# Kernel optimization log

Measured on AMD Instinct MI355X. Metric: run time of the kernel, lower is better.

The kernel has to match this reference:

```python
import jax, jax.numpy as jnp
import numpy as np

N, NFEAT, NHID, NCLASS, NHEAD = 8192, 512, 64, 16, 4
ALPHA = 0.1  # leaky relu slope
NEG = -9e15


def setup_inputs() -> dict:
    key = jax.random.key(0)
    ks = jax.random.split(key, 7)
    x = jax.random.normal(ks[0], (N, NFEAT), dtype=jnp.float32)
    adj = (jax.random.uniform(ks[1], (N, N)) < 0.05).astype(jnp.float32)
    # per-head params: W [H, nfeat, nhid], a [H, 2*nhid] (xavier-ish scale)
    W = jax.random.normal(ks[2], (NHEAD, NFEAT, NHID), dtype=jnp.float32) * (1.0 / np.sqrt(NFEAT))
    a = jax.random.normal(ks[3], (NHEAD, 2 * NHID), dtype=jnp.float32) * (1.0 / np.sqrt(NHID))
    W_out = jax.random.normal(ks[4], (NHEAD * NHID, NCLASS), dtype=jnp.float32) * (1.0 / np.sqrt(NHEAD * NHID))
    a_out = jax.random.normal(ks[5], (2 * NCLASS,), dtype=jnp.float32) * (1.0 / np.sqrt(NCLASS))
    return {"x": x, "adj": adj, "W": W, "a": a, "W_out": W_out, "a_out": a_out}


def _gat_layer(h, adj, Wk, ak):
    """Dense pyGAT GraphAttentionLayer (eval mode, dropout = identity)."""
    d = Wk.shape[1]
    Wh = h @ Wk                         # [N, d]
    f1 = Wh @ ak[:d]                    # [N]
    f2 = Wh @ ak[d:]                    # [N]
    e = jax.nn.leaky_relu(f1[:, None] + f2[None, :], negative_slope=ALPHA)  # [N, N]
    att = jax.nn.softmax(jnp.where(adj > 0, e, NEG), axis=1)
    return att @ Wh                     # [N, d]


def reference(x, adj, W, a, W_out, a_out):
    # eval mode: F.dropout is identity
    heads = jax.vmap(lambda Wk, ak: jax.nn.elu(_gat_layer(x, adj, Wk, ak)))(W, a)  # [H, N, nhid]
    h = jnp.transpose(heads, (1, 0, 2)).reshape(x.shape[0], -1)                    # [N, H*nhid]
    out = jax.nn.elu(_gat_layer(h, adj, W_out, a_out))                             # [N, nclass]
    return jax.nn.log_softmax(out, axis=1)
```

## Files before the change

### kernel.cpp

```cpp
#include <hip/hip_runtime.h>
#include <hip/hip_bf16.h>

#define NN 8192
#define NFEAT 512
#define NHID 64
#define NCLASS 16
#define NHEAD 4
#define ALPHA 0.1f
#define CAP 768

typedef short bf16x8 __attribute__((ext_vector_type(8)));
typedef float f32x4 __attribute__((ext_vector_type(4)));
typedef float fv4 __attribute__((ext_vector_type(4)));

__device__ __forceinline__ float lrelu(float x) { return fmaxf(x, ALPHA * x); }
__device__ __forceinline__ float elu(float x) { return x > 0.f ? x : __expf(x) - 1.f; }
__device__ __forceinline__ short f2b(float x) {
  union { __bf16 b; short s; } c; c.b = (__bf16)x; return c.s;
}
__device__ __forceinline__ float b2f(short x) {
  union { unsigned int u; float f; } c; c.u = ((unsigned int)(unsigned short)x) << 16; return c.f;
}

#define UPF(w, v, A0, A1)                                  \
  {                                                        \
    const float lo_ = __uint_as_float((v) << 16);          \
    const float hi_ = __uint_as_float((v) & 0xffff0000u);  \
    (A0) += (w) * lo_;                                     \
    (A1) += (w) * hi_;                                     \
  }

__global__ __launch_bounds__(256) void k_wprep(const float* __restrict__ W,
                                               short* __restrict__ WB) {
  __shared__ float t[64][65];
  const int h = blockIdx.y;
  const int k0 = blockIdx.x * 64;
  const int tid = threadIdx.x;
#pragma unroll
  for (int it = 0; it < 16; ++it) {
    const int r = it * 4 + (tid >> 6), c = tid & 63;
    t[r][c] = W[((size_t)h * NFEAT + k0 + r) * NHID + c];
  }
  __syncthreads();
#pragma unroll
  for (int it = 0; it < 16; ++it) {
    const int d = it * 4 + (tid >> 6), k = tid & 63;
    WB[((size_t)h * NHID + d) * NFEAT + k0 + k] = f2b(t[k][d]);
  }
}

__global__ __launch_bounds__(256) void k_prep1(const float* __restrict__ x,
                                               const short* __restrict__ WB,
                                               const float* __restrict__ a,
                                               short* __restrict__ Whf,
                                               float* __restrict__ f1i,
                                               float* __restrict__ f2i) {
  __shared__ short tile[64][72];
  const int bid = blockIdx.x;
  const int h = bid >> 7;
  const int bm = (bid & 127) * 64;
  const int tid = threadIdx.x;
  const int wv = tid >> 6, lane = tid & 63;
  const int mr = lane & 15, kg = lane >> 4;
  f32x4 acc0 = {0.f, 0.f, 0.f, 0.f}, acc1 = acc0, acc2 = acc0, acc3 = acc0;
  const float* ap = x + (size_t)(bm + wv * 16 + mr) * NFEAT + kg * 8;
  const short* bp = WB + ((size_t)h * NHID + mr) * NFEAT + kg * 8;
#pragma unroll 2
  for (int k0 = 0; k0 < NFEAT; k0 += 32) {
    const float4 xa = *reinterpret_cast<const float4*>(ap);
    const float4 xb = *reinterpret_cast<const float4*>(ap + 4);
    bf16x8 af;
    af[0] = f2b(xa.x); af[1] = f2b(xa.y); af[2] = f2b(xa.z); af[3] = f2b(xa.w);
    af[4] = f2b(xb.x); af[5] = f2b(xb.y); af[6] = f2b(xb.z); af[7] = f2b(xb.w);
    const bf16x8 b0 = *reinterpret_cast<const bf16x8*>(bp);
    const bf16x8 b1 = *reinterpret_cast<const bf16x8*>(bp + 16 * NFEAT);
    const bf16x8 b2 = *reinterpret_cast<const bf16x8*>(bp + 32 * NFEAT);
    const bf16x8 b3 = *reinterpret_cast<const bf16x8*>(bp + 48 * NFEAT);
    acc0 = __builtin_amdgcn_mfma_f32_16x16x32_bf16(af, b0, acc0, 0, 0, 0);
    acc1 = __builtin_amdgcn_mfma_f32_16x16x32_bf16(af, b1, acc1, 0, 0, 0);
    acc2 = __builtin_amdgcn_mfma_f32_16x16x32_bf16(af, b2, acc2, 0, 0, 0);
    acc3 = __builtin_amdgcn_mfma_f32_16x16x32_bf16(af, b3, acc3, 0, 0, 0);
    ap += 32; bp += 32;
  }
  float a1v[4], a2v[4];
#pragma unroll
  for (int c = 0; c < 4; ++c) {
    a1v[c] = a[h * 128 + mr + c * 16];
    a2v[c] = a[h * 128 + 64 + mr + c * 16];
  }
#pragma unroll
  for (int q = 0; q < 4; ++q) {
    float s1 = acc0[q] * a1v[0] + acc1[q] * a1v[1] + acc2[q] * a1v[2] + acc3[q] * a1v[3];
    float s2 = acc0[q] * a2v[0] + acc1[q] * a2v[1] + acc2[q] * a2v[2] + acc3[q] * a2v[3];
#pragma unroll
    for (int off = 1; off < 16; off <<= 1) {
      s1 += __shfl_xor(s1, off);
      s2 += __shfl_xor(s2, off);
    }
    if (mr == 0) {
      const int i = bm + wv * 16 + kg * 4 + q;
      f1i[(size_t)i * 4 + h] = s1;
      f2i[(size_t)i * 4 + h] = s2;
    }
  }
#pragma unroll
  for (int q = 0; q < 4; ++q) {
    const int r = wv * 16 + kg * 4 + q;
    tile[r][mr +  0] = f2b(acc0[q]);
    tile[r][mr + 16] = f2b(acc1[q]);
    tile[r][mr + 32] = f2b(acc2[q]);
    tile[r][mr + 48] = f2b(acc3[q]);
  }
  __syncthreads();
#pragma unroll
  for (int it = 0; it < 2; ++it) {
    const int jbl = (tid >> 6) + it * 4;
    const int d = tid & 63;
    bf16x8 o;
#pragma unroll
    for (int jo = 0; jo < 8; ++jo) o[jo] = tile[jbl * 8 + jo][d];
    *reinterpret_cast<bf16x8*>(Whf +
        (((size_t)h * 1024 + (bm >> 3) + jbl) * 64 + d) * 8) = o;
  }
}

__global__ __launch_bounds__(256) void k_rmax(const float* __restrict__ src,
                                              float* __restrict__ dst, int n, int stride,
                                              int boff) {
  const float* p = src + (size_t)blockIdx.x * boff;
  float m = -1e30f;
  for (int k = threadIdx.x; k < n; k += 256) m = fmaxf(m, p[(size_t)k * stride]);
#pragma unroll
  for (int off = 32; off; off >>= 1) m = fmaxf(m, __shfl_xor(m, off));
  __shared__ float sm[4];
  if ((threadIdx.x & 63) == 0) sm[threadIdx.x >> 6] = m;
  __syncthreads();
  if (threadIdx.x == 0) dst[blockIdx.x] = fmaxf(fmaxf(sm[0], sm[1]), fmaxf(sm[2], sm[3]));
}

__global__ __launch_bounds__(256) void k_acbd(const float* __restrict__ f1i,
                                              const float* __restrict__ f2i,
                                              const float* __restrict__ f2max,
                                              float2* __restrict__ ACh,
                                              unsigned int* __restrict__ BDh) {
  const int idx = blockIdx.x * 256 + threadIdx.x;
  const int i = idx & (NN - 1);
  const int h = idx >> 13;
  const float fm = f2max[h];
  const float f1 = f1i[(size_t)i * 4 + h];
  const float f2 = f2i[(size_t)i * 4 + h];
  const float s = f1 + fm;
  const float mrow = fmaxf(s, 0.1f * s);
  float2 ac;
  ac.x = __expf(s - mrow);
  ac.y = __expf(0.1f * s - mrow);
  ACh[(size_t)h * NN + i] = ac;
  const float t = f2 - fm;
  const unsigned int B = (unsigned short)f2b(__expf(t));
  const unsigned int D = (unsigned short)f2b(__expf(0.1f * t));
  BDh[(size_t)h * NN + i] = B | (D << 16);
}

__global__ __launch_bounds__(256) void k_scan(const float* __restrict__ adj,
                                              unsigned int* __restrict__ bmask) {
  const fv4* a4 = reinterpret_cast<const fv4*>(adj);
  const int t0 = blockIdx.x * 256 + threadIdx.x;
#pragma unroll 4
  for (int it = 0; it < 32; ++it) {
    const int g = it * 524288 + t0;
    const fv4 v = __builtin_nontemporal_load(a4 + g);
    unsigned int nv = (unsigned int)((v.x > 0.f) | ((v.y > 0.f) << 1) |
                                     ((v.z > 0.f) << 2) | ((v.w > 0.f) << 3))
                      << ((threadIdx.x & 7) * 4);
    nv |= __shfl_xor(nv, 1);
    nv |= __shfl_xor(nv, 2);
    nv |= __shfl_xor(nv, 4);
    if ((threadIdx.x & 7) == 0) bmask[g >> 3] = nv;
  }
}

#define DCH 512
__global__ __launch_bounds__(256) void k_dense1(const unsigned int* __restrict__ bmask,
                                                const short* __restrict__ Whf,
                                                const float2* __restrict__ ACh,
                                                const unsigned int* __restrict__ BDh,
                                                short* __restrict__ hcat) {
  __shared__ unsigned int sm_mask[64][16];
  __shared__ unsigned int sm_bd[DCH];
  __shared__ float sm_iv[4][16];
  __shared__ short sm_out[64][72];
  const int i0 = blockIdx.x * 64;
  const int h = blockIdx.y;
  const int tid = threadIdx.x;
  const int wv = tid >> 6, lane = tid & 63;
  const int mr = lane & 15, kg = lane >> 4;
  const int row_local = wv * 16 + mr;
  const float2 ac = ACh[(size_t)h * NN + i0 + row_local];
  f32x4 acc0 = {0.f, 0.f, 0.f, 0.f}, acc1 = acc0, acc2 = acc0, acc3 = acc0;
  float rs = 0.f;
  const int rr = tid >> 2, w0 = (tid & 3) * 4;

  for (int jc = 0; jc < NN; jc += DCH) {
    __syncthreads();
    {
      const unsigned int* src = bmask + (size_t)(i0 + rr) * 256 + (jc >> 5);
#pragma unroll
      for (int u = 0; u < 4; ++u) sm_mask[rr][w0 + u] = src[w0 + u];
      sm_bd[tid] = BDh[(size_t)h * NN + jc + tid];
      sm_bd[tid + 256] = BDh[(size_t)h * NN + jc + tid + 256];
    }
    __syncthreads();
#pragma unroll 4
    for (int ks = 0; ks < DCH / 32; ++ks) {
      const int jl = ks * 32 + kg * 8;
      const uint4 bda = *reinterpret_cast<const uint4*>(&sm_bd[jl]);
      const uint4 bdb = *reinterpret_cast<const uint4*>(&sm_bd[jl + 4]);
      const unsigned int mb = (sm_mask[row_local][ks] >> (kg * 8)) & 0xffu;
      bf16x8 af;
#define MKW(e, bdw)                                              \
      {                                                          \
        const float Bf = __uint_as_float((bdw) << 16);           \
        const float Df = __uint_as_float((bdw) & 0xffff0000u);   \
        float w_ = fmaxf(ac.x * Bf, ac.y * Df);                  \
        w_ = ((mb >> (e)) & 1u) ? w_ : 0.f;                      \
        rs += w_;                                                \
        af[e] = f2b(w_);                                         \
      }
      MKW(0, bda.x) MKW(1, bda.y) MKW(2, bda.z) MKW(3, bda.w)
      MKW(4, bdb.x) MKW(5, bdb.y) MKW(6, bdb.z) MKW(7, bdb.w)
#undef MKW
      const short* wp = Whf + (((size_t)h * 1024 + ((jc + jl) >> 3)) * 64 + mr) * 8;
      const bf16x8 bf0 = *reinterpret_cast<const bf16x8*>(wp);
      const bf16x8 bf1 = *reinterpret_cast<const bf16x8*>(wp + 128);
      const bf16x8 bf2 = *reinterpret_cast<const bf16x8*>(wp + 256);
      const bf16x8 bf3 = *reinterpret_cast<const bf16x8*>(wp + 384);
      acc0 = __builtin_amdgcn_mfma_f32_16x16x32_bf16(af, bf0, acc0, 0, 0, 0);
      acc1 = __builtin_amdgcn_mfma_f32_16x16x32_bf16(af, bf1, acc1, 0, 0, 0);
      acc2 = __builtin_amdgcn_mfma_f32_16x16x32_bf16(af, bf2, acc2, 0, 0, 0);
      acc3 = __builtin_amdgcn_mfma_f32_16x16x32_bf16(af, bf3, acc3, 0, 0, 0);
    }
  }
  rs += __shfl_xor(rs, 16);
  rs += __shfl_xor(rs, 32);
  if (lane < 16) sm_iv[wv][lane] = 1.f / rs;
  __syncthreads();
#pragma unroll
  for (int q = 0; q < 4; ++q) {
    const float ivq = sm_iv[wv][kg * 4 + q];
    const int r = wv * 16 + kg * 4 + q;
    sm_out[r][mr +  0] = f2b(elu(acc0[q] * ivq));
    sm_out[r][mr + 16] = f2b(elu(acc1[q] * ivq));
    sm_out[r][mr + 32] = f2b(elu(acc2[q] * ivq));
    sm_out[r][mr + 48] = f2b(elu(acc3[q] * ivq));
  }
  __syncthreads();
  {
    const int r = tid >> 2, seg = tid & 3;
    bf16x8 o;
#pragma unroll
    for (int u = 0; u < 8; ++u) o[u] = sm_out[r][seg * 16 + u];
    short* dst = hcat + (size_t)(i0 + r) * 256 + h * 64 + seg * 16;
    *reinterpret_cast<bf16x8*>(dst) = o;
    bf16x8 o2;
#pragma unroll
    for (int u = 0; u < 8; ++u) o2[u] = sm_out[r][seg * 16 + 8 + u];
    *reinterpret_cast<bf16x8*>(dst + 8) = o2;
  }
}

__global__ __launch_bounds__(256) void k_gemm2(const short* __restrict__ hcat,
                                               const float* __restrict__ Wout,
                                               const float* __restrict__ aout,
                                               short* __restrict__ Wh2B,
                                               float* __restrict__ f1o,
                                               float* __restrict__ f2o) {
  __shared__ float sW[NHEAD * NHID][NCLASS + 1];
  __shared__ float sh[16][NHEAD * NHID + 1];
  const int tid = threadIdx.x;
  const int r = tid >> 4, c = tid & 15;
  const int row = blockIdx.x * 16 + r;
  for (int u = tid; u < 256 * 16; u += 256) sW[u >> 4][u & 15] = Wout[u];
  for (int u = tid; u < 16 * 256; u += 256)
    sh[u >> 8][u & 255] = b2f(hcat[(size_t)(blockIdx.x * 16 + (u >> 8)) * 256 + (u & 255)]);
  __syncthreads();
  float acc = 0.f;
#pragma unroll 8
  for (int f = 0; f < 256; ++f) acc += sh[r][f] * sW[f][c];
  Wh2B[(size_t)row * NCLASS + c] = f2b(acc);
  float s1 = acc * aout[c];
  float s2 = acc * aout[NCLASS + c];
#pragma unroll
  for (int off = 8; off; off >>= 1) { s1 += __shfl_xor(s1, off); s2 += __shfl_xor(s2, off); }
  if (c == 0) { f1o[row] = s1; f2o[row] = s2; }
}

__global__ __launch_bounds__(256) void k_attn2(const unsigned int* __restrict__ bmask,
                                               const short* __restrict__ Wh2B,
                                               const float* __restrict__ f1o,
                                               const float* __restrict__ f2o,
                                               const float* __restrict__ f2omax,
                                               float* __restrict__ out) {
  __shared__ unsigned short idx[CAP];
  __shared__ unsigned int wj[CAP + 4];
  __shared__ float red[4][NCLASS];
  __shared__ float swp[4];
  __shared__ float sinvs;
  __shared__ int cnt;
  const int i = blockIdx.x;
  const int tid = threadIdx.x;
  const int wv = tid >> 6, lane = tid & 63;
  if (tid == 0) cnt = 0;
  __syncthreads();

  {
    unsigned int word = bmask[(size_t)i * 256 + tid];
    const int c = __popc(word);
    if (c) {
      int base = atomicAdd(&cnt, c);
      const int j0 = tid * 32;
      while (word) {
        const int b = __ffs(word) - 1;
        word &= word - 1;
        if (base < CAP) idx[base++] = (unsigned short)(j0 + b);
      }
    }
  }
  __syncthreads();
  const int n = min(cnt, CAP);
  if (tid < 4) wj[n + tid] = 0;

  const float f1r = f1o[i];
  const float mrow = lrelu(f1r + f2omax[0]);
  float sw = 0.f;
  for (int k = tid; k < n; k += 256) {
    const int j = idx[k];
    const float w = __expf(lrelu(f1r + f2o[j]) - mrow);
    wj[k] = ((unsigned int)(unsigned short)f2b(w) << 16) | (unsigned int)j;
    sw += w;
  }
#pragma unroll
  for (int off = 32; off; off >>= 1) sw += __shfl_xor(sw, off);
  if (lane == 0) swp[wv] = sw;
  __syncthreads();
  if (tid == 0) sinvs = 1.f / (swp[0] + swp[1] + swp[2] + swp[3]);
  __syncthreads();

  const int grp = tid >> 2, gl = tid & 3;
  float acc0 = 0.f, acc1 = 0.f, acc2 = 0.f, acc3 = 0.f;
  const short* wb = Wh2B + gl * 4;
  for (int kb = grp * 4; kb < n; kb += 256) {
    const uint4 pw = *reinterpret_cast<const uint4*>(wj + kb);
    const uint2 e0 = *reinterpret_cast<const uint2*>(wb + (size_t)(pw.x & 0xffffu) * NCLASS);
    const uint2 e1 = *reinterpret_cast<const uint2*>(wb + (size_t)(pw.y & 0xffffu) * NCLASS);
    const uint2 e2 = *reinterpret_cast<const uint2*>(wb + (size_t)(pw.z & 0xffffu) * NCLASS);
    const uint2 e3 = *reinterpret_cast<const uint2*>(wb + (size_t)(pw.w & 0xffffu) * NCLASS);
    const float w0 = __uint_as_float(pw.x & 0xffff0000u);
    const float w1 = __uint_as_float(pw.y & 0xffff0000u);
    const float w2 = __uint_as_float(pw.z & 0xffff0000u);
    const float w3 = __uint_as_float(pw.w & 0xffff0000u);
    UPF(w0, e0.x, acc0, acc1) UPF(w0, e0.y, acc2, acc3)
    UPF(w1, e1.x, acc0, acc1) UPF(w1, e1.y, acc2, acc3)
    UPF(w2, e2.x, acc0, acc1) UPF(w2, e2.y, acc2, acc3)
    UPF(w3, e3.x, acc0, acc1) UPF(w3, e3.y, acc2, acc3)
  }
  acc0 += __shfl_xor(acc0, 4);  acc1 += __shfl_xor(acc1, 4);
  acc2 += __shfl_xor(acc2, 4);  acc3 += __shfl_xor(acc3, 4);
  acc0 += __shfl_xor(acc0, 8);  acc1 += __shfl_xor(acc1, 8);
  acc2 += __shfl_xor(acc2, 8);  acc3 += __shfl_xor(acc3, 8);
  acc0 += __shfl_xor(acc0, 16); acc1 += __shfl_xor(acc1, 16);
  acc2 += __shfl_xor(acc2, 16); acc3 += __shfl_xor(acc3, 16);
  acc0 += __shfl_xor(acc0, 32); acc1 += __shfl_xor(acc1, 32);
  acc2 += __shfl_xor(acc2, 32); acc3 += __shfl_xor(acc3, 32);
  if (lane < 4) {
    red[wv][lane * 4 + 0] = acc0;
    red[wv][lane * 4 + 1] = acc1;
    red[wv][lane * 4 + 2] = acc2;
    red[wv][lane * 4 + 3] = acc3;
  }
  __syncthreads();
  if (tid < NCLASS) {
    const float s = red[0][tid] + red[1][tid] + red[2][tid] + red[3][tid];
    const float v = elu(s * sinvs);
    float vm = v;
#pragma unroll
    for (int off = 8; off; off >>= 1) vm = fmaxf(vm, __shfl_xor(vm, off, 16));
    float ex = __expf(v - vm);
#pragma unroll
    for (int off = 8; off; off >>= 1) ex += __shfl_xor(ex, off, 16);
    out[(size_t)i * NCLASS + tid] = v - vm - __logf(ex);
  }
}

extern "C" void kernel_launch(void* const* d_in, const int* in_sizes, int n_in,
                              void* d_out, int out_size, void* d_ws, size_t ws_size,
                              hipStream_t stream) {
  const float* x    = (const float*)d_in[0];
  const float* adj  = (const float*)d_in[1];
  const float* W    = (const float*)d_in[2];
  const float* a    = (const float*)d_in[3];
  const float* Wout = (const float*)d_in[4];
  const float* aout = (const float*)d_in[5];
  float* out = (float*)d_out;
  char* ws = (char*)d_ws;
  const size_t MB = 1048576;
  const size_t KB = 1024;

  unsigned int* bmask  = (unsigned int*)(ws);
  short* Whf           = (short*)(ws + 8 * MB);
  short* hcat          = (short*)(ws + 12 * MB);
  short* WB            = (short*)(ws + 16 * MB);
  float* f1i           = (float*)(ws + 16 * MB + 256 * KB);
  float* f2i           = (float*)(ws + 16 * MB + 384 * KB);
  float2* ACh          = (float2*)(ws + 16 * MB + 512 * KB);
  unsigned int* BDh    = (unsigned int*)(ws + 16 * MB + 768 * KB);
  float* f1o           = (float*)(ws + 16 * MB + 896 * KB);
  float* f2o           = (float*)(ws + 16 * MB + 928 * KB);
  short* Wh2B          = (short*)(ws + 16 * MB + 960 * KB);
  float* f2max         = (float*)(ws + 16 * MB + 1216 * KB);
  float* f2omax        = (float*)(ws + 16 * MB + 1216 * KB + 64);

  k_wprep<<<dim3(8, 4), 256, 0, stream>>>(W, WB);
  k_prep1<<<512, 256, 0, stream>>>(x, WB, a, Whf, f1i, f2i);
  k_rmax<<<NHEAD, 256, 0, stream>>>(f2i, f2max, NN, 4, 1);
  k_acbd<<<NN * NHEAD / 256, 256, 0, stream>>>(f1i, f2i, f2max, ACh, BDh);
  k_scan<<<2048, 256, 0, stream>>>(adj, bmask);
  k_dense1<<<dim3(NN / 64, NHEAD), 256, 0, stream>>>(bmask, Whf, ACh, BDh, hcat);
  k_gemm2<<<NN / 16, 256, 0, stream>>>(hcat, Wout, aout, Wh2B, f1o, f2o);
  k_rmax<<<1, 256, 0, stream>>>(f2o, f2omax, NN, 1, 0);
  k_attn2<<<NN, 256, 0, stream>>>(bmask, Wh2B, f1o, f2o, f2omax, out);
}
```

Before: 221.9 us.

## Fuse adjacency bitmask scan into first-layer attention kernel with per-head waves

Merges the separate adjacency-to-bitmask scan into the layer-1 attention kernel: each block now owns 16 rows, builds their bitmask from the fp32 adjacency in shared memory (also writing it out for layer 2), and assigns one wave per head instead of one block per head. This removes a kernel launch and the re-read of the bitmask, and shares the mask across the four heads. In exchange, blocks shrink to 16 rows, so the same Whf/BD tile is reused across fewer rows, BD is read directly from global instead of staged in LDS, and the adjacency read now sits serialized ahead of the MFMA loop inside each block.

```diff
diff --git a/kernel.cpp b/kernel.cpp
--- a/kernel.cpp
+++ b/kernel.cpp
@@ -161,110 +161,98 @@
   BDh[(size_t)h * NN + i] = B | (D << 16);
 }
 
-__global__ __launch_bounds__(256) void k_scan(const float* __restrict__ adj,
-                                              unsigned int* __restrict__ bmask) {
-  const fv4* a4 = reinterpret_cast<const fv4*>(adj);
-  const int t0 = blockIdx.x * 256 + threadIdx.x;
-#pragma unroll 4
-  for (int it = 0; it < 32; ++it) {
-    const int g = it * 524288 + t0;
-    const fv4 v = __builtin_nontemporal_load(a4 + g);
-    unsigned int nv = (unsigned int)((v.x > 0.f) | ((v.y > 0.f) << 1) |
-                                     ((v.z > 0.f) << 2) | ((v.w > 0.f) << 3))
-                      << ((threadIdx.x & 7) * 4);
-    nv |= __shfl_xor(nv, 1);
-    nv |= __shfl_xor(nv, 2);
-    nv |= __shfl_xor(nv, 4);
-    if ((threadIdx.x & 7) == 0) bmask[g >> 3] = nv;
-  }
-}
-
-#define DCH 512
-__global__ __launch_bounds__(256) void k_dense1(const unsigned int* __restrict__ bmask,
-                                                const short* __restrict__ Whf,
-                                                const float2* __restrict__ ACh,
-                                                const unsigned int* __restrict__ BDh,
-                                                short* __restrict__ hcat) {
-  __shared__ unsigned int sm_mask[64][16];
-  __shared__ unsigned int sm_bd[DCH];
+__global__ __launch_bounds__(256) void k_dense1f(const float* __restrict__ adj,
+                                                 const short* __restrict__ Whf,
+                                                 const float2* __restrict__ ACh,
+                                                 const unsigned int* __restrict__ BDh,
+                                                 short* __restrict__ hcat,
+                                                 unsigned int* __restrict__ bmask) {
+  __shared__ unsigned int sm_mask[16][257];
   __shared__ float sm_iv[4][16];
-  __shared__ short sm_out[64][72];
-  const int i0 = blockIdx.x * 64;
-  const int h = blockIdx.y;
+  __shared__ short sm_out[16][264];
+  const int i0 = blockIdx.x * 16;
   const int tid = threadIdx.x;
   const int wv = tid >> 6, lane = tid & 63;
   const int mr = lane & 15, kg = lane >> 4;
-  const int row_local = wv * 16 + mr;
-  const float2 ac = ACh[(size_t)h * NN + i0 + row_local];
+
+  {
+    const int row = tid >> 4, seg = tid & 15;
+    const fv4* a4 = reinterpret_cast<const fv4*>(adj) + (size_t)(i0 + row) * 2048 + seg * 128;
+    unsigned int* brow = bmask + (size_t)(i0 + row) * 256 + seg * 16;
+#pragma unroll 2
+    for (int w = 0; w < 16; ++w) {
+      unsigned int nv = 0;
+#pragma unroll
+      for (int q = 0; q < 8; ++q) {
+        const fv4 v = __builtin_nontemporal_load(a4 + w * 8 + q);
+        nv |= ((unsigned int)(v.x > 0.f) | ((unsigned int)(v.y > 0.f) << 1) |
+               ((unsigned int)(v.z > 0.f) << 2) | ((unsigned int)(v.w > 0.f) << 3))
+              << (q * 4);
+      }
+      sm_mask[row][seg * 16 + w] = nv;
+      brow[w] = nv;
+    }
+  }
+  __syncthreads();
+
+  const float2 ac = ACh[(size_t)wv * NN + i0 + mr];
   f32x4 acc0 = {0.f, 0.f, 0.f, 0.f}, acc1 = acc0, acc2 = acc0, acc3 = acc0;
   float rs = 0.f;
-  const int rr = tid >> 2, w0 = (tid & 3) * 4;
-
-  for (int jc = 0; jc < NN; jc += DCH) {
-    __syncthreads();
-    {
-      const unsigned int* src = bmask + (size_t)(i0 + rr) * 256 + (jc >> 5);
-#pragma unroll
-      for (int u = 0; u < 4; ++u) sm_mask[rr][w0 + u] = src[w0 + u];
-      sm_bd[tid] = BDh[(size_t)h * NN + jc + tid];
-      sm_bd[tid + 256] = BDh[(size_t)h * NN + jc + tid + 256];
-    }
-    __syncthreads();
-#pragma unroll 4
-    for (int ks = 0; ks < DCH / 32; ++ks) {
-      const int jl = ks * 32 + kg * 8;
-      const uint4 bda = *reinterpret_cast<const uint4*>(&sm_bd[jl]);
-      const uint4 bdb = *reinterpret_cast<const uint4*>(&sm_bd[jl + 4]);
-      const unsigned int mb = (sm_mask[row_local][ks] >> (kg * 8)) & 0xffu;
-      bf16x8 af;
+  const unsigned int* bdh = BDh + (size_t)wv * NN;
+  const short* whf = Whf + (size_t)wv * 1024 * 64 * 8 + (size_t)mr * 8;
+#pragma unroll 2
+  for (int ks = 0; ks < 256; ++ks) {
+    const int j = ks * 32 + kg * 8;
+    const unsigned int mb = (sm_mask[mr][ks] >> (kg * 8)) & 0xffu;
+    const uint4 bda = *reinterpret_cast<const uint4*>(bdh + j);
+    const uint4 bdb = *reinterpret_cast<const uint4*>(bdh + j + 4);
+    bf16x8 af;
 #define MKW(e, bdw)                                              \
-      {                                                          \
-        const float Bf = __uint_as_float((bdw) << 16);           \
-        const float Df = __uint_as_float((bdw) & 0xffff0000u);   \
-        float w_ = fmaxf(ac.x * Bf, ac.y * Df);                  \
-        w_ = ((mb >> (e)) & 1u) ? w_ : 0.f;                      \
-        rs += w_;                                                \
-        af[e] = f2b(w_);                                         \
-      }
-      MKW(0, bda.x) MKW(1, bda.y) MKW(2, bda.z) MKW(3, bda.w)
-      MKW(4, bdb.x) MKW(5, bdb.y) MKW(6, bdb.z) MKW(7, bdb.w)
+    {                                                            \
+      const float Bf = __uint_as_float((bdw) << 16);             \
+      const float Df = __uint_as_float((bdw) & 0xffff0000u);     \
+      float w_ = fmaxf(ac.x * Bf, ac.y * Df);                    \
+      w_ = ((mb >> (e)) & 1u) ? w_ : 0.f;                        \
+      rs += w_;                                                  \
+      af[e] = f2b(w_);                                           \
+    }
+    MKW(0, bda.x) MKW(1, bda.y) MKW(2, bda.z) MKW(3, bda.w)
+    MKW(4, bdb.x) MKW(5, bdb.y) MKW(6, bdb.z) MKW(7, bdb.w)
 #undef MKW
-      const short* wp = Whf + (((size_t)h * 1024 + ((jc + jl) >> 3)) * 64 + mr) * 8;
-      const bf16x8 bf0 = *reinterpret_cast<const bf16x8*>(wp);
-      const bf16x8 bf1 = *reinterpret_cast<const bf16x8*>(wp + 128);
-      const bf16x8 bf2 = *reinterpret_cast<const bf16x8*>(wp + 256);
-      const bf16x8 bf3 = *reinterpret_cast<const bf16x8*>(wp + 384);
-      acc0 = __builtin_amdgcn_mfma_f32_16x16x32_bf16(af, bf0, acc0, 0, 0, 0);
-      acc1 = __builtin_amdgcn_mfma_f32_16x16x32_bf16(af, bf1, acc1, 0, 0, 0);
-      acc2 = __builtin_amdgcn_mfma_f32_16x16x32_bf16(af, bf2, acc2, 0, 0, 0);
-      acc3 = __builtin_amdgcn_mfma_f32_16x16x32_bf16(af, bf3, acc3, 0, 0, 0);
-    }
+    const short* wp = whf + (size_t)(j >> 3) * 512;
+    const bf16x8 bf0 = *reinterpret_cast<const bf16x8*>(wp);
+    const bf16x8 bf1 = *reinterpret_cast<const bf16x8*>(wp + 128);
+    const bf16x8 bf2 = *reinterpret_cast<const bf16x8*>(wp + 256);
+    const bf16x8 bf3 = *reinterpret_cast<const bf16x8*>(wp + 384);
+    acc0 = __builtin_amdgcn_mfma_f32_16x16x32_bf16(af, bf0, acc0, 0, 0, 0);
+    acc1 = __builtin_amdgcn_mfma_f32_16x16x32_bf16(af, bf1, acc1, 0, 0, 0);
+    acc2 = __builtin_amdgcn_mfma_f32_16x16x32_bf16(af, bf2, acc2, 0, 0, 0);
+    acc3 = __builtin_amdgcn_mfma_f32_16x16x32_bf16(af, bf3, acc3, 0, 0, 0);
   }
   rs += __shfl_xor(rs, 16);
   rs += __shfl_xor(rs, 32);
   if (lane < 16) sm_iv[wv][lane] = 1.f / rs;
-  __syncthreads();
 #pragma unroll
   for (int q = 0; q < 4; ++q) {
     const float ivq = sm_iv[wv][kg * 4 + q];
-    const int r = wv * 16 + kg * 4 + q;
-    sm_out[r][mr +  0] = f2b(elu(acc0[q] * ivq));
-    sm_out[r][mr + 16] = f2b(elu(acc1[q] * ivq));
-    sm_out[r][mr + 32] = f2b(elu(acc2[q] * ivq));
-    sm_out[r][mr + 48] = f2b(elu(acc3[q] * ivq));
+    const int r = kg * 4 + q;
+    sm_out[r][wv * 64 + mr +  0] = f2b(elu(acc0[q] * ivq));
+    sm_out[r][wv * 64 + mr + 16] = f2b(elu(acc1[q] * ivq));
+    sm_out[r][wv * 64 + mr + 32] = f2b(elu(acc2[q] * ivq));
+    sm_out[r][wv * 64 + mr + 48] = f2b(elu(acc3[q] * ivq));
   }
   __syncthreads();
   {
-    const int r = tid >> 2, seg = tid & 3;
-    bf16x8 o;
-#pragma unroll
-    for (int u = 0; u < 8; ++u) o[u] = sm_out[r][seg * 16 + u];
-    short* dst = hcat + (size_t)(i0 + r) * 256 + h * 64 + seg * 16;
-    *reinterpret_cast<bf16x8*>(dst) = o;
-    bf16x8 o2;
-#pragma unroll
-    for (int u = 0; u < 8; ++u) o2[u] = sm_out[r][seg * 16 + 8 + u];
-    *reinterpret_cast<bf16x8*>(dst + 8) = o2;
+    const int row = tid >> 4, sgo = (tid & 15) * 16;
+    bf16x8 o0, o1;
+#pragma unroll
+    for (int u = 0; u < 8; ++u) {
+      o0[u] = sm_out[row][sgo + u];
+      o1[u] = sm_out[row][sgo + 8 + u];
+    }
+    short* dst = hcat + (size_t)(i0 + row) * 256 + sgo;
+    *reinterpret_cast<bf16x8*>(dst) = o0;
+    *reinterpret_cast<bf16x8*>(dst + 8) = o1;
   }
 }
 
@@ -423,8 +411,7 @@
   k_prep1<<<512, 256, 0, stream>>>(x, WB, a, Whf, f1i, f2i);
   k_rmax<<<NHEAD, 256, 0, stream>>>(f2i, f2max, NN, 4, 1);
   k_acbd<<<NN * NHEAD / 256, 256, 0, stream>>>(f1i, f2i, f2max, ACh, BDh);
-  k_scan<<<2048, 256, 0, stream>>>(adj, bmask);
-  k_dense1<<<dim3(NN / 64, NHEAD), 256, 0, stream>>>(bmask, Whf, ACh, BDh, hcat);
+  k_dense1f<<<NN / 16, 256, 0, stream>>>(adj, Whf, ACh, BDh, hcat, bmask);
   k_gemm2<<<NN / 16, 256, 0, stream>>>(hcat, Wout, aout, Wh2B, f1o, f2o);
   k_rmax<<<1, 256, 0, stream>>>(f2o, f2omax, NN, 1, 0);
   k_attn2<<<NN, 256, 0, stream>>>(bmask, Wh2B, f1o, f2o, f2omax, out);
```

Result: slower. 312.7 us (+40.9%).

## Split dense layer-1 attention along the neighbor axis with a combine kernel

Applied to the files above, without the earlier changes.

The layer-1 dense attention kernel is split into ZSPLIT=4 chunks along the column (neighbor) dimension via a third grid axis. Each chunk writes fp32 partial numerators and row sums to workspace, and a new combine kernel sums the partials, normalizes, applies ELU and writes bf16 hcat. This raises the block count from 512 to 2048 to better fill the GPU's compute units. The cost is 32 MB of extra partial-output traffic and one more kernel launch.

```diff
diff --git a/kernel.cpp b/kernel.cpp
--- a/kernel.cpp
+++ b/kernel.cpp
@@ -8,6 +8,9 @@
 #define NHEAD 4
 #define ALPHA 0.1f
 #define CAP 768
+#define ZSPLIT 4
+#define JPB (NN / ZSPLIT)
+#define DCH 512
 
 typedef short bf16x8 __attribute__((ext_vector_type(8)));
 typedef float f32x4 __attribute__((ext_vector_type(4)));
@@ -179,18 +182,18 @@
   }
 }
 
-#define DCH 512
-__global__ __launch_bounds__(256) void k_dense1(const unsigned int* __restrict__ bmask,
-                                                const short* __restrict__ Whf,
-                                                const float2* __restrict__ ACh,
-                                                const unsigned int* __restrict__ BDh,
-                                                short* __restrict__ hcat) {
+__global__ __launch_bounds__(256) void k_dense1z(const unsigned int* __restrict__ bmask,
+                                                 const short* __restrict__ Whf,
+                                                 const float2* __restrict__ ACh,
+                                                 const unsigned int* __restrict__ BDh,
+                                                 float* __restrict__ OpP,
+                                                 float* __restrict__ rsP) {
   __shared__ unsigned int sm_mask[64][16];
   __shared__ unsigned int sm_bd[DCH];
-  __shared__ float sm_iv[4][16];
-  __shared__ short sm_out[64][72];
   const int i0 = blockIdx.x * 64;
   const int h = blockIdx.y;
+  const int z = blockIdx.z;
+  const int jb0 = z * JPB;
   const int tid = threadIdx.x;
   const int wv = tid >> 6, lane = tid & 63;
   const int mr = lane & 15, kg = lane >> 4;
@@ -200,7 +203,7 @@
   float rs = 0.f;
   const int rr = tid >> 2, w0 = (tid & 3) * 4;
 
-  for (int jc = 0; jc < NN; jc += DCH) {
+  for (int jc = jb0; jc < jb0 + JPB; jc += DCH) {
     __syncthreads();
     {
       const unsigned int* src = bmask + (size_t)(i0 + rr) * 256 + (jc >> 5);
@@ -242,30 +245,33 @@
   }
   rs += __shfl_xor(rs, 16);
   rs += __shfl_xor(rs, 32);
-  if (lane < 16) sm_iv[wv][lane] = 1.f / rs;
-  __syncthreads();
+  if (lane < 16)
+    rsP[((size_t)z * NHEAD + h) * NN + i0 + wv * 16 + lane] = rs;
+  float* op = OpP + (((size_t)z * NHEAD + h) * NN + i0) * 64;
 #pragma unroll
   for (int q = 0; q < 4; ++q) {
-    const float ivq = sm_iv[wv][kg * 4 + q];
     const int r = wv * 16 + kg * 4 + q;
-    sm_out[r][mr +  0] = f2b(elu(acc0[q] * ivq));
-    sm_out[r][mr + 16] = f2b(elu(acc1[q] * ivq));
-    sm_out[r][mr + 32] = f2b(elu(acc2[q] * ivq));
-    sm_out[r][mr + 48] = f2b(elu(acc3[q] * ivq));
-  }
-  __syncthreads();
-  {
-    const int r = tid >> 2, seg = tid & 3;
-    bf16x8 o;
-#pragma unroll
-    for (int u = 0; u < 8; ++u) o[u] = sm_out[r][seg * 16 + u];
-    short* dst = hcat + (size_t)(i0 + r) * 256 + h * 64 + seg * 16;
-    *reinterpret_cast<bf16x8*>(dst) = o;
-    bf16x8 o2;
-#pragma unroll
-    for (int u = 0; u < 8; ++u) o2[u] = sm_out[r][seg * 16 + 8 + u];
-    *reinterpret_cast<bf16x8*>(dst + 8) = o2;
-  }
+    op[(size_t)r * 64 + mr +  0] = acc0[q];
+    op[(size_t)r * 64 + mr + 16] = acc1[q];
+    op[(size_t)r * 64 + mr + 32] = acc2[q];
+    op[(size_t)r * 64 + mr + 48] = acc3[q];
+  }
+}
+
+__global__ __launch_bounds__(256) void k_comb1(const float* __restrict__ OpP,
+                                               const float* __restrict__ rsP,
+                                               short* __restrict__ hcat) {
+  const int idx = blockIdx.x * 256 + threadIdx.x;
+  const int i = idx >> 8;
+  const int hc = idx & 255;
+  const int h = hc >> 6, d = hc & 63;
+  float s = 0.f, rsum = 0.f;
+#pragma unroll
+  for (int z = 0; z < ZSPLIT; ++z) {
+    s += OpP[(((size_t)z * NHEAD + h) * NN + i) * 64 + d];
+    rsum += rsP[((size_t)z * NHEAD + h) * NN + i];
+  }
+  hcat[idx] = f2b(elu(s / rsum));
 }
 
 __global__ __launch_bounds__(256) void k_gemm2(const short* __restrict__ hcat,
@@ -408,23 +414,26 @@
   unsigned int* bmask  = (unsigned int*)(ws);
   short* Whf           = (short*)(ws + 8 * MB);
   short* hcat          = (short*)(ws + 12 * MB);
-  short* WB            = (short*)(ws + 16 * MB);
-  float* f1i           = (float*)(ws + 16 * MB + 256 * KB);
-  float* f2i           = (float*)(ws + 16 * MB + 384 * KB);
-  float2* ACh          = (float2*)(ws + 16 * MB + 512 * KB);
-  unsigned int* BDh    = (unsigned int*)(ws + 16 * MB + 768 * KB);
-  float* f1o           = (float*)(ws + 16 * MB + 896 * KB);
-  float* f2o           = (float*)(ws + 16 * MB + 928 * KB);
-  short* Wh2B          = (short*)(ws + 16 * MB + 960 * KB);
-  float* f2max         = (float*)(ws + 16 * MB + 1216 * KB);
-  float* f2omax        = (float*)(ws + 16 * MB + 1216 * KB + 64);
+  float* OpP           = (float*)(ws + 16 * MB);
+  float* rsP           = (float*)(ws + 48 * MB);
+  short* WB            = (short*)(ws + 49 * MB);
+  float* f1i           = (float*)(ws + 49 * MB + 256 * KB);
+  float* f2i           = (float*)(ws + 49 * MB + 384 * KB);
+  float2* ACh          = (float2*)(ws + 49 * MB + 512 * KB);
+  unsigned int* BDh    = (unsigned int*)(ws + 49 * MB + 768 * KB);
+  float* f1o           = (float*)(ws + 49 * MB + 896 * KB);
+  float* f2o           = (float*)(ws + 49 * MB + 928 * KB);
+  short* Wh2B          = (short*)(ws + 49 * MB + 960 * KB);
+  float* f2max         = (float*)(ws + 49 * MB + 1216 * KB);
+  float* f2omax        = (float*)(ws + 49 * MB + 1216 * KB + 64);
 
   k_wprep<<<dim3(8, 4), 256, 0, stream>>>(W, WB);
   k_prep1<<<512, 256, 0, stream>>>(x, WB, a, Whf, f1i, f2i);
   k_rmax<<<NHEAD, 256, 0, stream>>>(f2i, f2max, NN, 4, 1);
   k_acbd<<<NN * NHEAD / 256, 256, 0, stream>>>(f1i, f2i, f2max, ACh, BDh);
   k_scan<<<2048, 256, 0, stream>>>(adj, bmask);
-  k_dense1<<<dim3(NN / 64, NHEAD), 256, 0, stream>>>(bmask, Whf, ACh, BDh, hcat);
+  k_dense1z<<<dim3(NN / 64, NHEAD, ZSPLIT), 256, 0, stream>>>(bmask, Whf, ACh, BDh, OpP, rsP);
+  k_comb1<<<NN, 256, 0, stream>>>(OpP, rsP, hcat);
   k_gemm2<<<NN / 16, 256, 0, stream>>>(hcat, Wout, aout, Wh2B, f1o, f2o);
   k_rmax<<<1, 256, 0, stream>>>(f2o, f2omax, NN, 1, 0);
   k_attn2<<<NN, 256, 0, stream>>>(bmask, Wh2B, f1o, f2o, f2omax, out);
```

After: 226.7 us. 2.2% more time.
